# Kernel tuning notes

Measured on AMD Instinct MI355X. Metric: run time of the kernel, lower is better.

## Reference

```python
import jax, jax.numpy as jnp
import numpy as np

B, N, M, C1, C2 = 8, 8192, 2048, 64, 128
MLP = [128, 128]
EPS = 1e-5


def setup_inputs() -> dict:
    key = jax.random.key(0)
    ks = jax.random.split(key, 12)
    inp = {
        'low_theta': jax.random.normal(ks[0], (B, N), jnp.float32),
        'low_phi': jax.random.normal(ks[1], (B, N), jnp.float32),
        'low_feats': jax.random.normal(ks[2], (B, C1, N), jnp.float32),
        'high_theta': jax.random.normal(ks[3], (B, M), jnp.float32),
        'high_phi': jax.random.normal(ks[4], (B, M), jnp.float32),
        'high_feats': jax.random.normal(ks[5], (B, C2, M), jnp.float32),
    }
    in_ch = C1 + C2
    # layer 0: conv1d (kernel size 1) -> weight [out, in], bias [out]; BN gamma/beta
    inp['W0'] = jax.random.normal(ks[6], (MLP[0], in_ch), jnp.float32) * 0.05
    inp['b0'] = jnp.zeros((MLP[0],), jnp.float32)
    inp['g0'] = jnp.ones((MLP[0],), jnp.float32)
    inp['beta0'] = jnp.zeros((MLP[0],), jnp.float32)
    # layer 1
    inp['W1'] = jax.random.normal(ks[7], (MLP[1], MLP[0]), jnp.float32) * 0.05
    inp['b1'] = jnp.zeros((MLP[1],), jnp.float32)
    inp['g1'] = jnp.ones((MLP[1],), jnp.float32)
    inp['beta1'] = jnp.zeros((MLP[1],), jnp.float32)
    return inp


def _conv_bn_relu(x, W, b, gamma, beta):
    # x: [B, Cin, N] -> 1x1 conv -> BN (training-mode batch stats, biased var) -> ReLU
    y = jnp.einsum('oi,bin->bon', W, x) + b[None, :, None]
    mean = jnp.mean(y, axis=(0, 2), keepdims=True)
    var = jnp.mean((y - mean) ** 2, axis=(0, 2), keepdims=True)
    yhat = (y - mean) * jax.lax.rsqrt(var + EPS)
    return jax.nn.relu(gamma[None, :, None] * yhat + beta[None, :, None])


def reference(low_theta, low_phi, low_feats, high_theta, high_phi, high_feats,
              W0, b0, g0, beta0, W1, b1, g1, beta1):
    # pairwise angular distance [B, N, M]
    dtheta = low_theta[:, :, None] - high_theta[:, None, :]
    dphi = low_phi[:, :, None] - high_phi[:, None, :]
    dist = jnp.sqrt(dtheta ** 2 + dphi ** 2)
    idx = jnp.argmin(dist, axis=-1)  # [B, N]
    # gather nearest-neighbor high features -> [B, C2, N]
    c2 = high_feats.shape[1]
    interpolated = jnp.take_along_axis(
        high_feats, jnp.broadcast_to(idx[:, None, :], (idx.shape[0], c2, idx.shape[1])), axis=2)
    cat = jnp.concatenate([low_feats, interpolated], axis=1)  # [B, C1+C2, N]
    h = _conv_bn_relu(cat, W0, b0, g0, beta0)
    out = _conv_bn_relu(h, W1, b1, g1, beta1)
    return out
```

## Files before the change

kernel.cpp:

```cpp
#include <hip/hip_runtime.h>
#include <hip/hip_bf16.h>

#define BB 8
#define NN 8192
#define MM 2048
#define C1 64
#define C2 128
#define CIN 192
#define CO 128
#define NB (BB*NN)
#define EPS 1e-5f

typedef unsigned short u16;
typedef unsigned int u32;
typedef __bf16 bf16_t;
typedef bf16_t bf16x8 __attribute__((ext_vector_type(8)));
typedef float f32x4 __attribute__((ext_vector_type(4)));

static __device__ __forceinline__ float b2f(u16 u) { return __uint_as_float(((u32)u) << 16); }
static __device__ __forceinline__ u16 f2b(float f) {
    __hip_bfloat16 h = __float2bfloat16(f);
    u16 u; __builtin_memcpy(&u, &h, 2); return u;
}

__global__ void k_prep_w(const float* __restrict__ W0, const float* __restrict__ W1,
                         u16* __restrict__ W0b, u16* __restrict__ W1b) {
    int t = blockIdx.x * 256 + threadIdx.x;
    if (t < CIN * CO) W0b[t] = f2b(W0[t]);
    if (t < CO * CO)  W1b[t] = f2b(W1[t]);
}

__global__ void k_prep_h(const float* __restrict__ hf, u16* __restrict__ hT) {
    __shared__ u16 s[64][65];
    int b = blockIdx.x, m0 = blockIdx.y * 64, c0 = blockIdx.z * 64;
    for (int e = threadIdx.x; e < 64 * 64; e += 256) {
        int i = e >> 6, j = e & 63;
        s[i][j] = f2b(hf[(b * C2 + c0 + i) * MM + m0 + j]);
    }
    __syncthreads();
    for (int e = threadIdx.x; e < 64 * 64; e += 256) {
        int ii = e & 63, jj = e >> 6;
        hT[(b * MM + m0 + jj) * C2 + c0 + ii] = s[ii][jj];
    }
}

__global__ __launch_bounds__(256) void k_argmin(
        const float* __restrict__ lt_, const float* __restrict__ lp_,
        const float* __restrict__ ht_, const float* __restrict__ hp_,
        int* __restrict__ idx) {
    __shared__ float2 hs[16 * 130];
    int b = blockIdx.x >> 8;
    int n0 = (blockIdx.x & 255) << 5;
    int tid = threadIdx.x;
    for (int e = tid; e < MM; e += 256) {
        int p = e >> 7, i = e & 127;
        hs[p * 130 + i] = make_float2(ht_[b * MM + e], hp_[b * MM + e]);
    }
    __syncthreads();
    int g = tid >> 4, p = tid & 15;
    int qbase = n0 + (g << 1);
    float lt0 = lt_[b * NN + qbase],     lp0 = lp_[b * NN + qbase];
    float lt1 = lt_[b * NN + qbase + 1], lp1 = lp_[b * NN + qbase + 1];
    float dl[2]  = {1e30f, 1e30f};
    float dpv[2] = {1e30f, 1e30f};
    int il[2] = {0, 0}, ipx[2] = {0, 0};
    const float2* hp2 = &hs[p * 130];
#pragma unroll 8
    for (int k = 0; k < 64; ++k) {
        f32x4 v = *(const f32x4*)&hp2[k * 2];
        {
            float dtA = lt0 - v[0], dpA = lp0 - v[1];
            float d2A = __fadd_rn(__fmul_rn(dtA, dtA), __fmul_rn(dpA, dpA));
            bool hA = d2A < dl[0];
            dpv[0] = hA ? dl[0] : dpv[0];
            ipx[0] = hA ? il[0] : ipx[0];
            dl[0]  = hA ? d2A : dl[0];
            il[0]  = hA ? (k * 2) : il[0];
            float dtB = lt0 - v[2], dpB = lp0 - v[3];
            float d2B = __fadd_rn(__fmul_rn(dtB, dtB), __fmul_rn(dpB, dpB));
            bool hB = d2B < dl[0];
            dpv[0] = hB ? dl[0] : dpv[0];
            ipx[0] = hB ? il[0] : ipx[0];
            dl[0]  = hB ? d2B : dl[0];
            il[0]  = hB ? (k * 2 + 1) : il[0];
        }
        {
            float dtA = lt1 - v[0], dpA = lp1 - v[1];
            float d2A = __fadd_rn(__fmul_rn(dtA, dtA), __fmul_rn(dpA, dpA));
            bool hA = d2A < dl[1];
            dpv[1] = hA ? dl[1] : dpv[1];
            ipx[1] = hA ? il[1] : ipx[1];
            dl[1]  = hA ? d2A : dl[1];
            il[1]  = hA ? (k * 2) : il[1];
            float dtB = lt1 - v[2], dpB = lp1 - v[3];
            float d2B = __fadd_rn(__fmul_rn(dtB, dtB), __fmul_rn(dpB, dpB));
            bool hB = d2B < dl[1];
            dpv[1] = hB ? dl[1] : dpv[1];
            ipx[1] = hB ? il[1] : ipx[1];
            dl[1]  = hB ? d2B : dl[1];
            il[1]  = hB ? (k * 2 + 1) : il[1];
        }
    }
    int mbase = p << 7;
#pragma unroll
    for (int j = 0; j < 2; ++j) {
        float sl = __fsqrt_rn(dl[j]);
        float sp = __fsqrt_rn(dpv[j]);
        int bm = mbase + ((sp == sl) ? ipx[j] : il[j]);
        float bs = sl;
#pragma unroll
        for (int d = 1; d <= 8; d <<= 1) {
            float ov = __shfl_xor(bs, d, 64);
            int om = __shfl_xor(bm, d, 64);
            if (ov < bs || (ov == bs && om < bm)) { bs = ov; bm = om; }
        }
        if (p == 0) idx[b * NN + qbase + j] = bm;
    }
}

static __device__ __forceinline__ void epilogue(
        f32x4* ac0, f32x4* ac1, const float* bias, u16* yl,
        float* chs, float* chq, int w, int ln, int q) {
#pragma unroll
    for (int mf = 0; mf < 2; ++mf) {
        f32x4* A = mf ? ac1 : ac0;
        int chb = 32 * w + 16 * mf + 4 * q;
        float bs[4], ss[4] = {0.f, 0.f, 0.f, 0.f}, sq[4] = {0.f, 0.f, 0.f, 0.f};
#pragma unroll
        for (int r = 0; r < 4; ++r) bs[r] = bias[chb + r];
#pragma unroll
        for (int nf = 0; nf < 4; ++nf) {
            int n = (nf << 4) + ln;
#pragma unroll
            for (int r = 0; r < 4; ++r) {
                float y = A[nf][r] + bs[r];
                ss[r] += y; sq[r] += y * y;
                int o = chb + r;
                yl[(o << 6) + (n ^ ((o & 7) << 3))] = f2b(y);
            }
        }
#pragma unroll
        for (int r = 0; r < 4; ++r) {
            float v = ss[r], u2 = sq[r];
#pragma unroll
            for (int d = 1; d < 16; d <<= 1) {
                v += __shfl_xor(v, d, 64);
                u2 += __shfl_xor(u2, d, 64);
            }
            if (ln == 0) { atomicAdd(&chs[chb + r], v); atomicAdd(&chq[chb + r], u2); }
        }
    }
}

__global__ __launch_bounds__(256) void k_red(const float* __restrict__ gpart,
                                             float* __restrict__ gout) {
    __shared__ float part[4];
    int c = blockIdx.x;
    int t = threadIdx.x;
    float s = 0.f;
#pragma unroll
    for (int k = 0; k < 4; ++k)
        s += gpart[(t + (k << 8)) * 256 + c];
#pragma unroll
    for (int d = 1; d < 64; d <<= 1)
        s += __shfl_xor(s, d, 64);
    if ((t & 63) == 0) part[t >> 6] = s;
    __syncthreads();
    if (t == 0) gout[c] = (part[0] + part[1]) + (part[2] + part[3]);
}

__global__ __launch_bounds__(256) void k_l0(
        const float* __restrict__ lf, const u16* __restrict__ hT, const int* __restrict__ idx,
        const u16* __restrict__ W0b, const float* __restrict__ b0,
        u16* __restrict__ y0, float* __restrict__ gpart) {
    __shared__ u16 xt[64 * CIN];
    __shared__ u16 ylds[CO * 64];
    __shared__ float chs[CO], chq[CO];
    __shared__ int idxs[64];
    int tid = threadIdx.x;
    int l = tid & 63, w = tid >> 6, ln = l & 15, q = l >> 4;
    int b = blockIdx.x >> 7, n0 = (blockIdx.x & 127) << 6;
    if (tid < 64) idxs[tid] = idx[b * NN + n0 + tid];
    if (tid < 128) { chs[tid] = 0.f; chq[tid] = 0.f; }
    __syncthreads();
    {
        const float* src = lf + (size_t)(b * C1 + l) * NN + n0 + (w << 4);
        float4 f0 = *(const float4*)src;
        float4 f1 = *(const float4*)(src + 4);
        float4 f2 = *(const float4*)(src + 8);
        float4 f3 = *(const float4*)(src + 12);
        float v[16] = {f0.x, f0.y, f0.z, f0.w, f1.x, f1.y, f1.z, f1.w,
                       f2.x, f2.y, f2.z, f2.w, f3.x, f3.y, f3.z, f3.w};
        int cc = l >> 3, clo = l & 7;
#pragma unroll
        for (int i = 0; i < 16; ++i) {
            int n = (w << 4) + i;
            xt[n * CIN + ((cc ^ (i & 7)) << 3) + clo] = f2b(v[i]);
        }
    }
    for (int e = tid; e < 1024; e += 256) {
        int n = e >> 4, c16 = e & 15;
        uint4 v = *(const uint4*)(hT + (size_t)(b * MM + idxs[n]) * C2 + (c16 << 3));
        *(uint4*)&xt[n * CIN + (((8 + c16) ^ (n & 7)) << 3)] = v;
    }
    __syncthreads();
    f32x4 ac0[4], ac1[4];
#pragma unroll
    for (int nf = 0; nf < 4; ++nf) {
        ac0[nf] = f32x4{0.f, 0.f, 0.f, 0.f};
        ac1[nf] = f32x4{0.f, 0.f, 0.f, 0.f};
    }
    const u16* w0r0 = W0b + (32 * w + ln) * CIN + 8 * q;
    const u16* w0r1 = w0r0 + 16 * CIN;
#pragma unroll
    for (int s = 0; s < 6; ++s) {
        bf16x8 a0 = *(const bf16x8*)(w0r0 + 32 * s);
        bf16x8 a1 = *(const bf16x8*)(w0r1 + 32 * s);
#pragma unroll
        for (int nf = 0; nf < 4; ++nf) {
            bf16x8 bv = *(const bf16x8*)&xt[(16 * nf + ln) * CIN + (((4 * s + q) ^ (ln & 7)) << 3)];
            ac0[nf] = __builtin_amdgcn_mfma_f32_16x16x32_bf16(a0, bv, ac0[nf], 0, 0, 0);
            ac1[nf] = __builtin_amdgcn_mfma_f32_16x16x32_bf16(a1, bv, ac1[nf], 0, 0, 0);
        }
    }
    epilogue(ac0, ac1, b0, ylds, chs, chq, w, ln, q);
    __syncthreads();
    gpart[blockIdx.x * 256 + tid] = (tid < 128) ? chs[tid] : chq[tid - 128];
    {
        int o = tid >> 1, h = tid & 1;
#pragma unroll
        for (int jj = 0; jj < 4; ++jj) {
            int j = (h << 2) + jj;
            uint4 v = *(const uint4*)&ylds[(o << 6) + ((j ^ (o & 7)) << 3)];
            *(uint4*)(y0 + (size_t)(b * CO + o) * NN + n0 + (j << 3)) = v;
        }
    }
}

__global__ __launch_bounds__(256) void k_l1(
        u16* __restrict__ y, const float* __restrict__ g0, const float* __restrict__ be0,
        const u16* __restrict__ W1b, const float* __restrict__ b1,
        const float* __restrict__ gstat, float* __restrict__ gpart) {
    __shared__ u16 xt[64 * CO];
    __shared__ u16 ylds[CO * 64];
    __shared__ float chs[CO], chq[CO], sc[CO], sh[CO];
    int tid = threadIdx.x;
    int l = tid & 63, w = tid >> 6, ln = l & 15, q = l >> 4;
    int b = blockIdx.x >> 7, n0 = (blockIdx.x & 127) << 6;
    if (tid < 128) {
        float s = gstat[tid], qv = gstat[128 + tid];
        float mu = s * (1.f / NB);
        float var = qv * (1.f / NB) - mu * mu;
        float istd = 1.f / __fsqrt_rn(var + EPS);
        float scale = g0[tid] * istd;
        sc[tid] = scale;
        sh[tid] = be0[tid] - mu * scale;
        chs[tid] = 0.f; chq[tid] = 0.f;
    }
    __syncthreads();
#pragma unroll
    for (int it = 0; it < 2; ++it) {
        int c = (it << 6) + l;
        const u16* src = y + (size_t)(b * CO + c) * NN + n0 + (w << 4);
        uint4 r0 = *(const uint4*)src;
        uint4 r1 = *(const uint4*)(src + 8);
        u16 raw[16];
        *(uint4*)&raw[0] = r0;
        *(uint4*)&raw[8] = r1;
        float scale = sc[c], shift = sh[c];
        int cc = c >> 3, clo = c & 7;
#pragma unroll
        for (int i = 0; i < 16; ++i) {
            int n = (w << 4) + i;
            float hv = fmaxf(b2f(raw[i]) * scale + shift, 0.f);
            xt[(n << 7) + ((cc ^ (i & 7)) << 3) + clo] = f2b(hv);
        }
    }
    __syncthreads();
    f32x4 ac0[4], ac1[4];
#pragma unroll
    for (int nf = 0; nf < 4; ++nf) {
        ac0[nf] = f32x4{0.f, 0.f, 0.f, 0.f};
        ac1[nf] = f32x4{0.f, 0.f, 0.f, 0.f};
    }
    const u16* w1r0 = W1b + (32 * w + ln) * CO + 8 * q;
    const u16* w1r1 = w1r0 + 16 * CO;
#pragma unroll
    for (int s = 0; s < 4; ++s) {
        bf16x8 a0 = *(const bf16x8*)(w1r0 + 32 * s);
        bf16x8 a1 = *(const bf16x8*)(w1r1 + 32 * s);
#pragma unroll
        for (int nf = 0; nf < 4; ++nf) {
            bf16x8 bv = *(const bf16x8*)&xt[((16 * nf + ln) << 7) + (((4 * s + q) ^ (ln & 7)) << 3)];
            ac0[nf] = __builtin_amdgcn_mfma_f32_16x16x32_bf16(a0, bv, ac0[nf], 0, 0, 0);
            ac1[nf] = __builtin_amdgcn_mfma_f32_16x16x32_bf16(a1, bv, ac1[nf], 0, 0, 0);
        }
    }
    epilogue(ac0, ac1, b1, ylds, chs, chq, w, ln, q);
    __syncthreads();
    gpart[blockIdx.x * 256 + tid] = (tid < 128) ? chs[tid] : chq[tid - 128];
    {
        int o = tid >> 1, h = tid & 1;
#pragma unroll
        for (int jj = 0; jj < 4; ++jj) {
            int j = (h << 2) + jj;
            uint4 v = *(const uint4*)&ylds[(o << 6) + ((j ^ (o & 7)) << 3)];
            *(uint4*)(y + (size_t)(b * CO + o) * NN + n0 + (j << 3)) = v;
        }
    }
}

__global__ __launch_bounds__(256) void k_bn1(
        const u16* __restrict__ y, const float* __restrict__ gstat,
        const float* __restrict__ g1, const float* __restrict__ be1,
        float* __restrict__ out) {
    int t = blockIdx.x * 256 + threadIdx.x;
    int o = (t >> 10) & 127;
    float s = gstat[256 + o], qv = gstat[384 + o];
    float mu = s * (1.f / NB);
    float var = qv * (1.f / NB) - mu * mu;
    float istd = 1.f / __fsqrt_rn(var + EPS);
    float scale = g1[o] * istd;
    float shift = be1[o] - mu * scale;
    size_t e0 = (size_t)t << 3;
    uint4 v = *(const uint4*)(y + e0);
    u16 raw[8];
    *(uint4*)raw = v;
    float r[8];
#pragma unroll
    for (int k = 0; k < 8; ++k)
        r[k] = fmaxf(b2f(raw[k]) * scale + shift, 0.f);
    *(float4*)(out + e0) = make_float4(r[0], r[1], r[2], r[3]);
    *(float4*)(out + e0 + 4) = make_float4(r[4], r[5], r[6], r[7]);
}

extern "C" void kernel_launch(void* const* d_in, const int* in_sizes, int n_in,
                              void* d_out, int out_size, void* d_ws, size_t ws_size,
                              hipStream_t stream) {
    const float* lt = (const float*)d_in[0];
    const float* lp = (const float*)d_in[1];
    const float* lf = (const float*)d_in[2];
    const float* ht = (const float*)d_in[3];
    const float* hp = (const float*)d_in[4];
    const float* hf = (const float*)d_in[5];
    const float* W0 = (const float*)d_in[6];
    const float* b0 = (const float*)d_in[7];
    const float* g0 = (const float*)d_in[8];
    const float* be0 = (const float*)d_in[9];
    const float* W1 = (const float*)d_in[10];
    const float* b1 = (const float*)d_in[11];
    const float* g1 = (const float*)d_in[12];
    const float* be1 = (const float*)d_in[13];

    char* ws = (char*)d_ws;
    u16* y0 = (u16*)ws;
    u16* hT = (u16*)(ws + 16777216);
    int* idx = (int*)(ws + 20971520);
    float* gstat = (float*)(ws + 21233664);
    u16* W0b = (u16*)(ws + 21235712);
    u16* W1b = (u16*)(ws + 21284864);
    float* gpart = (float*)(ws + 21317632);

    k_prep_w<<<96, 256, 0, stream>>>(W0, W1, W0b, W1b);
    k_prep_h<<<dim3(8, 32, 2), 256, 0, stream>>>(hf, hT);
    k_argmin<<<2048, 256, 0, stream>>>(lt, lp, ht, hp, idx);
    k_l0<<<1024, 256, 0, stream>>>(lf, hT, idx, W0b, b0, y0, gpart);
    k_red<<<256, 256, 0, stream>>>(gpart, gstat);
    k_l1<<<1024, 256, 0, stream>>>(y0, g0, be0, W1b, b1, gstat, gpart);
    k_red<<<256, 256, 0, stream>>>(gpart, gstat + 256);
    k_bn1<<<4096, 256, 0, stream>>>(y0, gstat, g1, be1, (float*)d_out);
}
```

Before: 107.8 us.

## Split argmin into min-distance pass and index recovery pass

The argmin kernel's main loop now tracks only the running minimum squared distances, using fminf in even and odd accumulators, and drops the per-candidate index and second-best bookkeeping. After a cross-lane min reduction, a ballot picks the lowest partition holding the minimum. The 16 lanes then rescan that partition's 128 candidates, comparing square-rooted distances to recover the lowest matching index. This cuts selects and register pressure in the hot loop at the cost of a small second pass. Tie-breaking on equal square roots is meant to keep the first-index semantics.

```diff
diff --git a/kernel.cpp b/kernel.cpp
--- a/kernel.cpp
+++ b/kernel.cpp
@@ -13,6 +13,7 @@
 
 typedef unsigned short u16;
 typedef unsigned int u32;
+typedef unsigned long long u64;
 typedef __bf16 bf16_t;
 typedef bf16_t bf16x8 __attribute__((ext_vector_type(8)));
 typedef float f32x4 __attribute__((ext_vector_type(4)));
@@ -58,63 +59,71 @@
     }
     __syncthreads();
     int g = tid >> 4, p = tid & 15;
+    int gw = (tid & 63) >> 4;
     int qbase = n0 + (g << 1);
     float lt0 = lt_[b * NN + qbase],     lp0 = lp_[b * NN + qbase];
     float lt1 = lt_[b * NN + qbase + 1], lp1 = lp_[b * NN + qbase + 1];
-    float dl[2]  = {1e30f, 1e30f};
-    float dpv[2] = {1e30f, 1e30f};
-    int il[2] = {0, 0}, ipx[2] = {0, 0};
     const float2* hp2 = &hs[p * 130];
+    float me0 = 1e30f, mo0 = 1e30f, me1 = 1e30f, mo1 = 1e30f;
 #pragma unroll 8
     for (int k = 0; k < 64; ++k) {
         f32x4 v = *(const f32x4*)&hp2[k * 2];
+        float dtA0 = lt0 - v[0], dpA0 = lp0 - v[1];
+        me0 = fminf(me0, __fadd_rn(__fmul_rn(dtA0, dtA0), __fmul_rn(dpA0, dpA0)));
+        float dtB0 = lt0 - v[2], dpB0 = lp0 - v[3];
+        mo0 = fminf(mo0, __fadd_rn(__fmul_rn(dtB0, dtB0), __fmul_rn(dpB0, dpB0)));
+        float dtA1 = lt1 - v[0], dpA1 = lp1 - v[1];
+        me1 = fminf(me1, __fadd_rn(__fmul_rn(dtA1, dtA1), __fmul_rn(dpA1, dpA1)));
+        float dtB1 = lt1 - v[2], dpB1 = lp1 - v[3];
+        mo1 = fminf(mo1, __fadd_rn(__fmul_rn(dtB1, dtB1), __fmul_rn(dpB1, dpB1)));
+    }
+    float sp0 = __fsqrt_rn(fminf(me0, mo0));
+    float sp1 = __fsqrt_rn(fminf(me1, mo1));
+    float s0 = sp0, s1 = sp1;
+#pragma unroll
+    for (int d = 1; d <= 8; d <<= 1) {
+        s0 = fminf(s0, __shfl_xor(s0, d, 64));
+        s1 = fminf(s1, __shfl_xor(s1, d, 64));
+    }
+    u64 bm0 = __ballot(sp0 == s0);
+    u64 bm1 = __ballot(sp1 == s1);
+    int P0 = __ffs((int)((bm0 >> (gw * 16)) & 0xffffULL)) - 1;
+    int P1 = __ffs((int)((bm1 >> (gw * 16)) & 0xffffULL)) - 1;
+    int f0 = 0x7fffffff, f1 = 0x7fffffff;
+    const float2* r0 = &hs[P0 * 130 + (p << 3)];
+    const float2* r1 = &hs[P1 * 130 + (p << 3)];
+#pragma unroll
+    for (int k = 0; k < 4; ++k) {
+        int kk = (k + p) & 3;
         {
+            f32x4 v = *(const f32x4*)&r0[kk * 2];
+            int lc = (p << 3) + (kk << 1);
             float dtA = lt0 - v[0], dpA = lp0 - v[1];
-            float d2A = __fadd_rn(__fmul_rn(dtA, dtA), __fmul_rn(dpA, dpA));
-            bool hA = d2A < dl[0];
-            dpv[0] = hA ? dl[0] : dpv[0];
-            ipx[0] = hA ? il[0] : ipx[0];
-            dl[0]  = hA ? d2A : dl[0];
-            il[0]  = hA ? (k * 2) : il[0];
+            float sA = __fsqrt_rn(__fadd_rn(__fmul_rn(dtA, dtA), __fmul_rn(dpA, dpA)));
+            f0 = min(f0, (sA == s0) ? lc : 0x7fffffff);
             float dtB = lt0 - v[2], dpB = lp0 - v[3];
-            float d2B = __fadd_rn(__fmul_rn(dtB, dtB), __fmul_rn(dpB, dpB));
-            bool hB = d2B < dl[0];
-            dpv[0] = hB ? dl[0] : dpv[0];
-            ipx[0] = hB ? il[0] : ipx[0];
-            dl[0]  = hB ? d2B : dl[0];
-            il[0]  = hB ? (k * 2 + 1) : il[0];
+            float sB = __fsqrt_rn(__fadd_rn(__fmul_rn(dtB, dtB), __fmul_rn(dpB, dpB)));
+            f0 = min(f0, (sB == s0) ? lc + 1 : 0x7fffffff);
         }
         {
+            f32x4 v = *(const f32x4*)&r1[kk * 2];
+            int lc = (p << 3) + (kk << 1);
             float dtA = lt1 - v[0], dpA = lp1 - v[1];
-            float d2A = __fadd_rn(__fmul_rn(dtA, dtA), __fmul_rn(dpA, dpA));
-            bool hA = d2A < dl[1];
-            dpv[1] = hA ? dl[1] : dpv[1];
-            ipx[1] = hA ? il[1] : ipx[1];
-            dl[1]  = hA ? d2A : dl[1];
-            il[1]  = hA ? (k * 2) : il[1];
+            float sA = __fsqrt_rn(__fadd_rn(__fmul_rn(dtA, dtA), __fmul_rn(dpA, dpA)));
+            f1 = min(f1, (sA == s1) ? lc : 0x7fffffff);
             float dtB = lt1 - v[2], dpB = lp1 - v[3];
-            float d2B = __fadd_rn(__fmul_rn(dtB, dtB), __fmul_rn(dpB, dpB));
-            bool hB = d2B < dl[1];
-            dpv[1] = hB ? dl[1] : dpv[1];
-            ipx[1] = hB ? il[1] : ipx[1];
-            dl[1]  = hB ? d2B : dl[1];
-            il[1]  = hB ? (k * 2 + 1) : il[1];
-        }
-    }
-    int mbase = p << 7;
-#pragma unroll
-    for (int j = 0; j < 2; ++j) {
-        float sl = __fsqrt_rn(dl[j]);
-        float sp = __fsqrt_rn(dpv[j]);
-        int bm = mbase + ((sp == sl) ? ipx[j] : il[j]);
-        float bs = sl;
-#pragma unroll
-        for (int d = 1; d <= 8; d <<= 1) {
-            float ov = __shfl_xor(bs, d, 64);
-            int om = __shfl_xor(bm, d, 64);
-            if (ov < bs || (ov == bs && om < bm)) { bs = ov; bm = om; }
-        }
-        if (p == 0) idx[b * NN + qbase + j] = bm;
+            float sB = __fsqrt_rn(__fadd_rn(__fmul_rn(dtB, dtB), __fmul_rn(dpB, dpB)));
+            f1 = min(f1, (sB == s1) ? lc + 1 : 0x7fffffff);
+        }
+    }
+#pragma unroll
+    for (int d = 1; d <= 8; d <<= 1) {
+        f0 = min(f0, __shfl_xor(f0, d, 64));
+        f1 = min(f1, __shfl_xor(f1, d, 64));
+    }
+    if (p == 0) {
+        idx[b * NN + qbase]     = (P0 << 7) + f0;
+        idx[b * NN + qbase + 1] = (P1 << 7) + f1;
     }
 }
 
```

Measured after the change: 96.37 us. -10.6%, faster.
